# Kernel tuning notes

Measured on AMD Instinct MI355X. Metric: run time of the kernel, lower is better.

## Reference

```python
import jax, jax.numpy as jnp
import numpy as np

N_RBF = 32
EPS_DIST = 0.01
R_RBF_MAX = 5.0
POWERS = (1.0, -1.0)


def _rbf_features(dist):
    # dist: [..., ] -> [..., N_RBF]; Gaussian-on-distance 'soft one-hot'
    q = jnp.linspace(0.0, 1.0, N_RBF).astype(dist.dtype)
    mu = q ** 2 * R_RBF_MAX
    sigma = (1.0 + R_RBF_MAX * q) / 7.0
    d = dist[..., None]
    return d ** 2 * jnp.exp(-d - ((d - mu) / sigma) ** 2)


def _pair_features(diff, dist):
    # RBF (32) + distance powers (2) + raw differences (3) = 37 features
    f_dist = jnp.stack(
        [dist ** n if n > 0 else 1.0 / (dist ** (-n) + EPS_DIST) for n in POWERS],
        axis=-1,
    )
    return jnp.concatenate([_rbf_features(dist), f_dist, diff], axis=-1)


def _mlp(x, Ws, bs):
    # MLP with linear_out=False: activation applied after every layer incl. last
    for W, b in zip(Ws, bs):
        x = jax.nn.silu(x @ W + b)
    return x


def setup_inputs() -> dict:
    key = jax.random.key(0)
    ks = jax.random.split(key, 6)
    B, N, M = 2048, 32, 8
    D_PAIR = N_RBF + 2 + 3  # 37
    H, F1, F_ION = 128, 128, 32
    r = jax.random.normal(ks[0], (B, N, 3), jnp.float32) * 2.0
    R = jax.random.normal(ks[1], (M, 3), jnp.float32) * 3.0
    Z = jnp.arange(1, M + 1, dtype=jnp.float32)
    init = lambda k, s: (jax.random.normal(k, s, jnp.float32) / np.sqrt(s[0])).astype(jnp.float32)
    return dict(
        r=r, R=R, Z=Z,
        W0=init(ks[2], (D_PAIR, H)), b0=jnp.zeros((H,), jnp.float32),
        W1=init(ks[3], (H, F1)), b1=jnp.zeros((F1,), jnp.float32),
        Wion=init(ks[4], (1, F_ION)), bion=jnp.zeros((F_ION,), jnp.float32),
    )


def reference(r, R, Z, W0, b0, W1, b1, Wion, bion):
    B, N = r.shape[0], r.shape[1]
    # --- pairwise diffs / distances ---
    diff_el_el = r[..., :, None, :] - r[..., None, :, :]          # [B,N,N,3]
    eye = jnp.eye(N, dtype=r.dtype)
    # safe sqrt on the diagonal (grad-safe), diagonal distance forced to 0
    dist_el_el = jnp.sqrt(jnp.sum(diff_el_el ** 2, axis=-1) + eye) * (1.0 - eye)  # [B,N,N]
    diff_el_ion = r[..., :, None, :] - R                           # [B,N,M,3]
    dist_el_ion = jnp.sqrt(jnp.sum(diff_el_ion ** 2, axis=-1))     # [B,N,M]

    # --- per-edge features ---
    features_el_el = _pair_features(diff_el_el, dist_el_el)        # [B,N,N,37]
    features_el_ion = _pair_features(diff_el_ion, dist_el_ion)     # [B,N,M,37]

    # --- edge MLP + sum aggregation over ions ---
    h = _mlp(features_el_ion, [W0, W1], [b0, b1])                  # [B,N,M,128]
    one_el = jnp.sum(h, axis=-2)                                   # [B,N,128]
    concat_ei = jnp.reshape(features_el_ion, features_el_ion.shape[:-2] + (-1,))  # [B,N,M*37]
    features_el = jnp.concatenate([one_el, concat_ei], axis=-1)    # [B,N,128+M*37]

    # --- ion features ---
    Zt = jnp.tile(Z, (B, 1))                                       # [B,M]
    features_ion = jax.nn.silu(Zt[..., None] @ Wion + bion)        # [B,M,32]
    return (features_el, features_ion)
```

## Files before the change

kernel.cpp:

```cpp
#include <hip/hip_runtime.h>


typedef __attribute__((ext_vector_type(8))) short short8;
typedef __attribute__((ext_vector_type(4))) float f32x4;

#define ITERS     8
#define UNITS_IT  16
#define ROWLEN    424
#define OUT_EL    27787264

__device__ __forceinline__ unsigned short f2bf(float f){
    unsigned int u = __builtin_bit_cast(unsigned int, f);
    u += 0x7fffu + ((u >> 16) & 1u);
    return (unsigned short)(u >> 16);
}
__device__ __forceinline__ unsigned int cvtpk_bf16(float lo, float hi){
    unsigned int r;
    asm("v_cvt_pk_bf16_f32 %0, %1, %2" : "=v"(r) : "v"(lo), "v"(hi));
    return r;
}
__device__ __forceinline__ unsigned short bf16s(float x){
    return (unsigned short)cvtpk_bf16(x, x);
}
__device__ __forceinline__ float fast_silu(float x){
    return x * __builtin_amdgcn_rcpf(1.0f + __expf(-x));
}

__global__ __launch_bounds__(512, 4)
void el_kernel(const float* __restrict__ r,
               const float* __restrict__ Rion,
               const float* __restrict__ W0,
               const float* __restrict__ b0,
               const float* __restrict__ W1,
               const float* __restrict__ b1,
               const float* __restrict__ Z,
               const float* __restrict__ Wion,
               const float* __restrict__ bion,
               float* __restrict__ out)
{
    __shared__ __align__(16) unsigned short W0L[8][2][64][8];
    __shared__ __align__(16) unsigned short W1L[8][4][64][8];
    __shared__ __align__(16) unsigned short UNI[8][1920];

    const int t    = threadIdx.x;
    const int lane = t & 63;
    const int w    = t >> 6;
    const int quad = lane >> 4;
    const int l16  = lane & 15;

    for (int i = t; i < 8*2*64*8; i += 512){
        int j = i & 7, ln = (i >> 3) & 63, ch = (i >> 9) & 1, tc = i >> 10;
        int q = ln >> 4, n = tc*16 + (ln & 15);
        float v = 0.f;
        if (ch == 0)            v = W0[(q*8 + j)*128 + n];
        else if (q == 0){
            if      (j < 5)     v = W0[(32 + j)*128 + n];
            else if (j == 5)    v = b0[n];
        }
        ((unsigned short*)W0L)[i] = f2bf(v);
    }
    for (int i = t; i < 8*4*64*8; i += 512){
        int j = i & 7, ln = (i >> 3) & 63, c = (i >> 9) & 3, tc = i >> 11;
        int k = c*32 + (ln >> 4)*8 + j, n = tc*16 + (ln & 15);
        ((unsigned short*)W1L)[i] = f2bf(W1[k*128 + n]);
    }
    if (t < 128){
        int ww = t >> 4, e = t & 15;
        #pragma unroll
        for (int b = 0; b < 2; ++b){
            UNI[ww][b*640 + 512 + e*8 + 5] = 0x3F80;
            UNI[ww][b*640 + 512 + e*8 + 6] = 0;
            UNI[ww][b*640 + 512 + e*8 + 7] = 0;
        }
    }

    {
        int e0 = (blockIdx.x*512 + t)*2;
        int j0 = e0 & 31, mm = (e0 >> 5) & 7;
        float z = Z[mm];
        float2 v;
        v.x = fast_silu(z * Wion[j0]     + bion[j0]);
        v.y = fast_silu(z * Wion[j0 + 1] + bion[j0 + 1]);
        *(float2*)&out[OUT_EL + e0] = v;
    }

    const int frow  = t >> 2;
    const int phase = t & 3;
    const int ul    = frow >> 3;
    const int m     = frow & 7;
    const int e16   = frow & 15;
    const float Rx = Rion[m*3+0];
    const float Ry = Rion[m*3+1];
    const float Rz = Rion[m*3+2];

    unsigned short* const uw = &UNI[w][0];

    const f32x4 zeroc = {0.f,0.f,0.f,0.f};

    float bias1[8];
    #pragma unroll
    for (int tc = 0; tc < 8; ++tc) bias1[tc] = b1[tc*16 + l16];

    float muA[8], isA[8];
    #pragma unroll
    for (int kk = 0; kk < 8; ++kk){
        float q = (float)(phase + 4*kk) * (1.0f/31.0f);
        muA[kk] = q*q*5.0f;
        isA[kk] = 7.0f * __builtin_amdgcn_rcpf(1.0f + 5.0f*q);
    }

    const int ubase0 = blockIdx.x * (UNITS_IT * ITERS);

    auto feat_pass = [&](int gu, int fb, float px, float py, float pz){
        float dx = px - Rx, dy = py - Ry, dz = pz - Rz;
        float d2 = dx*dx + dy*dy + dz*dz;
        float d  = __builtin_amdgcn_sqrtf(d2);
        float* orow = &out[(size_t)gu*ROWLEN + 128 + m*37];
        #pragma unroll
        for (int kk = 0; kk < 8; ++kk){
            float uu  = (d - muA[kk]) * isA[kk];
            float val = d2 * __expf(-d - uu*uu);
            orow[phase + 4*kk] = val;
            uw[fb + (kk >> 1)*128 + e16*8 + phase + ((kk & 1) << 2)] = bf16s(val);
        }
        float tv = (phase == 0) ? d :
                   (phase == 1) ? __builtin_amdgcn_rcpf(d + 0.01f) :
                   (phase == 2) ? dx : dy;
        orow[32 + phase] = tv;
        orow[36]         = dz;
        uw[fb + 512 + e16*8 + phase] = bf16s(tv);
        uw[fb + 512 + e16*8 + 4]     = bf16s(dz);
    };

    {
        int gu = ubase0 + ul;
        feat_pass(gu, 0, r[gu*3+0], r[gu*3+1], r[gu*3+2]);
    }
    float cx, cy, cz;
    {
        int gu = ubase0 + UNITS_IT + ul;
        cx = r[gu*3+0]; cy = r[gu*3+1]; cz = r[gu*3+2];
    }

    __syncthreads();

    int cur = 0;
    for (int it = 0; it < ITERS; ++it){
        const int ubase = ubase0 + it * UNITS_IT;

        int gun = ubase0 + (((it + 2) & (ITERS-1)) * UNITS_IT) + ul;
        float nx = r[gun*3+0], ny = r[gun*3+1], nz = r[gun*3+2];

        short8 bf0 = *(const short8*)&uw[cur + quad*128 + l16*8];
        short8 bf1 = *(const short8*)&uw[cur + 512 + l16*8];

        {
            int gu = ubase0 + (((it + 1) & (ITERS-1)) * UNITS_IT) + ul;
            feat_pass(gu, cur ^ 640, cx, cy, cz);
        }

        f32x4 acc1[8];
        #pragma unroll
        for (int i = 0; i < 8; ++i) acc1[i] = zeroc;

        #pragma unroll
        for (int c = 0; c < 4; ++c){
            #pragma unroll
            for (int h = 0; h < 2; ++h){
                const int tc = 2*c + h;
                short8 a0 = *(const short8*)&W0L[tc][0][lane][0];
                short8 a1 = *(const short8*)&W0L[tc][1][lane][0];
                f32x4 acc = __builtin_amdgcn_mfma_f32_16x16x32_bf16(a0, bf0, zeroc, 0, 0, 0);
                acc       = __builtin_amdgcn_mfma_f32_16x16x32_bf16(a1, bf1, acc,   0, 0, 0);
                unsigned int p01 = cvtpk_bf16(fast_silu(acc[0]), fast_silu(acc[1]));
                unsigned int p23 = cvtpk_bf16(fast_silu(acc[2]), fast_silu(acc[3]));
                unsigned long long pk = (unsigned long long)p01 |
                                        ((unsigned long long)p23 << 32);
                *(unsigned long long*)&uw[1280 + l16*40 + h*16 + quad*4] = pk;
            }
            short8 afk = *(const short8*)&uw[1280 + l16*40 + quad*8];
            __builtin_amdgcn_s_setprio(1);
            #pragma unroll
            for (int tc2 = 0; tc2 < 8; ++tc2){
                short8 bw = *(const short8*)&W1L[tc2][c][lane][0];
                acc1[tc2] = __builtin_amdgcn_mfma_f32_16x16x32_bf16(afk, bw, acc1[tc2], 0, 0, 0);
            }
            __builtin_amdgcn_s_setprio(0);
        }

        #pragma unroll
        for (int tc = 0; tc < 8; ++tc){
            float v = 0.f;
            #pragma unroll
            for (int rr = 0; rr < 4; ++rr) v += fast_silu(acc1[tc][rr] + bias1[tc]);
            v += __shfl_xor(v, 16, 64);
            if ((quad & 1) == 0){
                size_t gu = (size_t)(ubase + 2*w + (quad >> 1));
                out[gu*ROWLEN + tc*16 + l16] = v;
            }
        }

        cur ^= 640;
        cx = nx; cy = ny; cz = nz;
    }
}

extern "C" void kernel_launch(void* const* d_in, const int* in_sizes, int n_in,
                              void* d_out, int out_size, void* d_ws, size_t ws_size,
                              hipStream_t stream)
{
    const float* r    = (const float*)d_in[0];
    const float* Rion = (const float*)d_in[1];
    const float* Z    = (const float*)d_in[2];
    const float* W0   = (const float*)d_in[3];
    const float* b0   = (const float*)d_in[4];
    const float* W1   = (const float*)d_in[5];
    const float* b1   = (const float*)d_in[6];
    const float* Wion = (const float*)d_in[7];
    const float* bion = (const float*)d_in[8];
    float* out = (float*)d_out;

    el_kernel<<<dim3(512), dim3(512), 0, stream>>>(r, Rion, W0, b0, W1, b1,
                                                   Z, Wion, bion, out);
}
```

Before: 181.8 us.

## Move W1 out of LDS into a prepacked global buffer and raise occupancy

A separate prep kernel converts W1 to bf16 in MFMA fragment order in workspace. The main kernel then reads W1 fragments straight from global memory (served by cache) instead of staging them in LDS. This frees 32KB of LDS per block, so the launch bound goes from 4 to 6 blocks per CU. The grid also grows from 512 to 768 blocks with uneven 6/5 iteration splits to fill the CUs better. The cost is an extra kernel launch and per-MFMA global or L1 loads of W1 in the inner loop.

```diff
diff --git a/kernel.cpp b/kernel.cpp
--- a/kernel.cpp
+++ b/kernel.cpp
@@ -4,8 +4,6 @@
 typedef __attribute__((ext_vector_type(8))) short short8;
 typedef __attribute__((ext_vector_type(4))) float f32x4;
 
-#define ITERS     8
-#define UNITS_IT  16
 #define ROWLEN    424
 #define OUT_EL    27787264
 
@@ -26,20 +24,28 @@
     return x * __builtin_amdgcn_rcpf(1.0f + __expf(-x));
 }
 
-__global__ __launch_bounds__(512, 4)
+__global__ __launch_bounds__(256)
+void prep_w1(const float* __restrict__ W1, unsigned short* __restrict__ w1f)
+{
+    int i = blockIdx.x*256 + threadIdx.x;
+    int j = i & 7, ln = (i >> 3) & 63, c = (i >> 9) & 3, tc = i >> 11;
+    int k = c*32 + (ln >> 4)*8 + j, n = tc*16 + (ln & 15);
+    w1f[i] = f2bf(W1[k*128 + n]);
+}
+
+__global__ __launch_bounds__(512, 6)
 void el_kernel(const float* __restrict__ r,
                const float* __restrict__ Rion,
                const float* __restrict__ W0,
                const float* __restrict__ b0,
-               const float* __restrict__ W1,
                const float* __restrict__ b1,
+               const unsigned short* __restrict__ w1f,
                const float* __restrict__ Z,
                const float* __restrict__ Wion,
                const float* __restrict__ bion,
                float* __restrict__ out)
 {
     __shared__ __align__(16) unsigned short W0L[8][2][64][8];
-    __shared__ __align__(16) unsigned short W1L[8][4][64][8];
     __shared__ __align__(16) unsigned short UNI[8][1920];
 
     const int t    = threadIdx.x;
@@ -59,11 +65,6 @@
         }
         ((unsigned short*)W0L)[i] = f2bf(v);
     }
-    for (int i = t; i < 8*4*64*8; i += 512){
-        int j = i & 7, ln = (i >> 3) & 63, c = (i >> 9) & 3, tc = i >> 11;
-        int k = c*32 + (ln >> 4)*8 + j, n = tc*16 + (ln & 15);
-        ((unsigned short*)W1L)[i] = f2bf(W1[k*128 + n]);
-    }
     if (t < 128){
         int ww = t >> 4, e = t & 15;
         #pragma unroll
@@ -75,13 +76,16 @@
     }
 
     {
-        int e0 = (blockIdx.x*512 + t)*2;
-        int j0 = e0 & 31, mm = (e0 >> 5) & 7;
-        float z = Z[mm];
-        float2 v;
-        v.x = fast_silu(z * Wion[j0]     + bion[j0]);
-        v.y = fast_silu(z * Wion[j0 + 1] + bion[j0 + 1]);
-        *(float2*)&out[OUT_EL + e0] = v;
+        int tid = blockIdx.x*512 + t;
+        if (tid < 262144){
+            int e0 = tid*2;
+            int j0 = e0 & 31, mm = (e0 >> 5) & 7;
+            float z = Z[mm];
+            float2 v;
+            v.x = fast_silu(z * Wion[j0]     + bion[j0]);
+            v.y = fast_silu(z * Wion[j0 + 1] + bion[j0 + 1]);
+            *(float2*)&out[OUT_EL + e0] = v;
+        }
     }
 
     const int frow  = t >> 2;
@@ -109,7 +113,9 @@
         isA[kk] = 7.0f * __builtin_amdgcn_rcpf(1.0f + 5.0f*q);
     }
 
-    const int ubase0 = blockIdx.x * (UNITS_IT * ITERS);
+    const int bid    = blockIdx.x;
+    const int niter  = (bid < 256) ? 6 : 5;
+    const int ubase0 = (bid < 256) ? bid*96 : 24576 + (bid - 256)*80;
 
     auto feat_pass = [&](int gu, int fb, float px, float py, float pz){
         float dx = px - Rx, dy = py - Ry, dz = pz - Rz;
@@ -138,24 +144,29 @@
     }
     float cx, cy, cz;
     {
-        int gu = ubase0 + UNITS_IT + ul;
+        int gu = ubase0 + 16 + ul;
         cx = r[gu*3+0]; cy = r[gu*3+1]; cz = r[gu*3+2];
     }
 
     __syncthreads();
 
     int cur = 0;
-    for (int it = 0; it < ITERS; ++it){
-        const int ubase = ubase0 + it * UNITS_IT;
-
-        int gun = ubase0 + (((it + 2) & (ITERS-1)) * UNITS_IT) + ul;
+    for (int it = 0; it < niter; ++it){
+        const int ubase = ubase0 + it * 16;
+
+        const unsigned short* w1p = w1f;
+        asm volatile("" : "+s"(w1p));
+
+        int i2 = it + 2; if (i2 >= niter) i2 -= niter;
+        int gun = ubase0 + i2*16 + ul;
         float nx = r[gun*3+0], ny = r[gun*3+1], nz = r[gun*3+2];
 
         short8 bf0 = *(const short8*)&uw[cur + quad*128 + l16*8];
         short8 bf1 = *(const short8*)&uw[cur + 512 + l16*8];
 
         {
-            int gu = ubase0 + (((it + 1) & (ITERS-1)) * UNITS_IT) + ul;
+            int i1 = it + 1; if (i1 >= niter) i1 -= niter;
+            int gu = ubase0 + i1*16 + ul;
             feat_pass(gu, cur ^ 640, cx, cy, cz);
         }
 
@@ -181,9 +192,18 @@
             short8 afk = *(const short8*)&uw[1280 + l16*40 + quad*8];
             __builtin_amdgcn_s_setprio(1);
             #pragma unroll
-            for (int tc2 = 0; tc2 < 8; ++tc2){
-                short8 bw = *(const short8*)&W1L[tc2][c][lane][0];
-                acc1[tc2] = __builtin_amdgcn_mfma_f32_16x16x32_bf16(afk, bw, acc1[tc2], 0, 0, 0);
+            for (int g = 0; g < 2; ++g){
+                short8 bwv[4];
+                #pragma unroll
+                for (int u = 0; u < 4; ++u){
+                    int tc2 = g*4 + u;
+                    bwv[u] = *(const short8*)&w1p[tc2*2048 + c*512 + lane*8];
+                }
+                #pragma unroll
+                for (int u = 0; u < 4; ++u){
+                    int tc2 = g*4 + u;
+                    acc1[tc2] = __builtin_amdgcn_mfma_f32_16x16x32_bf16(afk, bwv[u], acc1[tc2], 0, 0, 0);
+                }
             }
             __builtin_amdgcn_s_setprio(0);
         }
@@ -219,7 +239,9 @@
     const float* Wion = (const float*)d_in[7];
     const float* bion = (const float*)d_in[8];
     float* out = (float*)d_out;
-
-    el_kernel<<<dim3(512), dim3(512), 0, stream>>>(r, Rion, W0, b0, W1, b1,
+    unsigned short* w1f = (unsigned short*)d_ws;
+
+    prep_w1<<<dim3(64), dim3(256), 0, stream>>>(W1, w1f);
+    el_kernel<<<dim3(768), dim3(512), 0, stream>>>(r, Rion, W0, b0, b1, w1f,
                                                    Z, Wion, bion, out);
 }
```

New measurement: 358.1 us. +97.0%, slower.
